# Kernel optimization log

Hardware: AMD Instinct MI355X
Metric: run time of the kernel (lower is better)

The kernel has to match this reference:

```python
import jax, jax.numpy as jnp
import numpy as np

N_NODES = 50000
N_EDGES = 800000
D = 128


def _degrees(idx, n):
    # in/out degree via segment_sum of ones, clamped to >=1 (DGL clamp)
    ones = jnp.ones(idx.shape[0], dtype=jnp.float32)
    return jnp.clip(jax.ops.segment_sum(ones, idx, num_segments=n), 1.0)


def graph_conv(x, src, dst, W, b):
    # DGL GraphConv, norm='both', aggregate-then-matmul (in_feats == out_feats)
    n = x.shape[0]
    deg_out = _degrees(src, n)  # [N]
    deg_in = _degrees(dst, n)   # [N]
    xs = x * jax.lax.rsqrt(deg_out)[:, None]          # [N, D] pre-normalize
    msg = jax.ops.segment_sum(xs[src], dst, num_segments=n)  # gather+scatter [N, D]
    h = msg * jax.lax.rsqrt(deg_in)[:, None]
    return h @ W + b


def setup_inputs() -> dict:
    key = jax.random.key(0)
    k1, k2, k3, k4, k5 = jax.random.split(key, 5)
    x = jax.random.normal(k1, (N_NODES, D), dtype=jnp.float32)
    src = jax.random.randint(k2, (N_EDGES,), 0, N_NODES, dtype=jnp.int64)
    dst = jax.random.randint(k3, (N_EDGES,), 0, N_NODES, dtype=jnp.int64)
    scale = 1.0 / np.sqrt(D)
    W1 = jax.random.normal(k4, (D, D), dtype=jnp.float32) * scale
    W2 = jax.random.normal(k5, (D, D), dtype=jnp.float32) * scale
    b1 = jnp.zeros((D,), dtype=jnp.float32)
    b2 = jnp.zeros((D,), dtype=jnp.float32)
    return {"x": x, "src": src, "dst": dst, "W1": W1, "b1": b1, "W2": W2, "b2": b2}


def reference(x, src, dst, W1, b1, W2, b2):
    h = graph_conv(x, src, dst, W1, b1)
    h = jax.nn.relu(h)
    return graph_conv(h, src, dst, W2, b2)
```

## Files before the change

### kernel.cpp

```cpp
#include <hip/hip_runtime.h>

#define N_NODES 50000
#define N_EDGES 800000
#define D 128
#define CAP 48
#define OVF_CAP 4096

#define BINS 40
#define PNODES 1250
#define B1 64
#define CH1 ((N_EDGES + B1 - 1) / B1)
#define NW (N_NODES / 4)

typedef unsigned short bf16_t;
typedef __attribute__((ext_vector_type(8))) short short8v;
typedef __attribute__((ext_vector_type(4))) float f32x4;

__device__ inline float bf2f(bf16_t u) {
    union { unsigned int i; float f; } v;
    v.i = ((unsigned int)u) << 16;
    return v.f;
}
__device__ inline bf16_t f2bf(float f) {
    union { float f; unsigned int i; } v;
    v.f = f;
    unsigned int u = v.i;
    unsigned int r = (u + 0x7FFFu + ((u >> 16) & 1u)) >> 16;
    return (bf16_t)r;
}
__device__ inline float u2f_lo(unsigned int u) {
    union { unsigned int i; float f; } x; x.i = u << 16; return x.f;
}
__device__ inline float u2f_hi(unsigned int u) {
    union { unsigned int i; float f; } x; x.i = u & 0xFFFF0000u; return x.f;
}


__global__ __launch_bounds__(1024) void hist40_kernel(const int* __restrict__ src,
                                                      const int* __restrict__ dst,
                                                      unsigned int* __restrict__ H40,
                                                      unsigned int* __restrict__ SH, int nE) {
    __shared__ unsigned int hb[BINS];
    __shared__ unsigned int hs[NW];
    for (int i = threadIdx.x; i < NW; i += 1024) hs[i] = 0u;
    if (threadIdx.x < BINS) hb[threadIdx.x] = 0u;
    __syncthreads();
    int e0 = blockIdx.x * CH1;
    int e1 = min(e0 + CH1, nE);
    for (int e = e0 + (int)threadIdx.x; e < e1; e += 1024) {
        int s = src[e];
        int d = dst[e];
        atomicAdd(&hs[s >> 2], 1u << (8 * (s & 3)));
        atomicAdd(&hb[d / PNODES], 1u);
    }
    __syncthreads();
    if (threadIdx.x < BINS) H40[blockIdx.x * BINS + threadIdx.x] = hb[threadIdx.x];
    unsigned int* SHb = SH + (size_t)blockIdx.x * NW;
    for (int i = threadIdx.x; i < NW; i += 1024) SHb[i] = hs[i];
}

__global__ void scan40_kernel(const unsigned int* __restrict__ H40,
                              unsigned int* __restrict__ OFF40,
                              unsigned int* __restrict__ binBase,
                              unsigned int* __restrict__ binTot) {
    __shared__ unsigned int part[B1 * BINS];
    __shared__ unsigned int tot[BINS], base[BINS];
    int j = (int)threadIdx.x;
    if (j < BINS) {
        unsigned int run = 0;
        for (int b = 0; b < B1; b++) {
            part[b * BINS + j] = run;
            run += H40[b * BINS + j];
        }
        tot[j] = run;
    }
    __syncthreads();
    if (j == 0) {
        unsigned int run = 0;
        for (int q = 0; q < BINS; q++) { base[q] = run; run += tot[q]; }
    }
    __syncthreads();
    if (j < BINS) {
        binBase[j] = base[j];
        binTot[j] = tot[j];
        for (int b = 0; b < B1; b++) OFF40[b * BINS + j] = part[b * BINS + j] + base[j];
    }
}

__global__ __launch_bounds__(1024) void place40_kernel(const int* __restrict__ src,
                                                       const int* __restrict__ dst,
                                                       const unsigned int* __restrict__ OFF40,
                                                       unsigned int* __restrict__ binned, int nE) {
    __shared__ unsigned int cur[BINS];
    if (threadIdx.x < BINS) cur[threadIdx.x] = OFF40[blockIdx.x * BINS + threadIdx.x];
    __syncthreads();
    int e0 = blockIdx.x * CH1;
    int e1 = min(e0 + CH1, nE);
    for (int e = e0 + (int)threadIdx.x; e < e1; e += 1024) {
        int s = src[e];
        int d = dst[e];
        int bin = d / PNODES;
        unsigned int pos = atomicAdd(&cur[bin], 1u);
        binned[pos] = (unsigned int)(d - bin * PNODES) | ((unsigned int)s << 16);
    }
}

__global__ void sreduce_kernel(const unsigned int* __restrict__ SH, int* __restrict__ cnt_s) {
    int w = blockIdx.x * 256 + (int)threadIdx.x;
    if (w >= NW) return;
    unsigned int run = 0;
#pragma unroll 8
    for (int b = 0; b < B1; b++) run += SH[(size_t)b * NW + w];
    int4 c;
    c.x = (int)(run & 0xFFu); c.y = (int)((run >> 8) & 0xFFu);
    c.z = (int)((run >> 16) & 0xFFu); c.w = (int)(run >> 24);
    ((int4*)cnt_s)[w] = c;
}

__global__ __launch_bounds__(1024) void scatter2_kernel(
    const unsigned int* __restrict__ binned, const unsigned int* __restrict__ binBase,
    const unsigned int* __restrict__ binTot, unsigned short* __restrict__ bucket,
    int* __restrict__ cnt_d, int* __restrict__ ovf_cnt, int2* __restrict__ ovf) {
    __shared__ unsigned short bk[PNODES * CAP];
    __shared__ unsigned int cur[PNODES];
    const int j = blockIdx.x;
    const int nbeg = j * PNODES;
    for (int i = threadIdx.x; i < PNODES; i += 1024) cur[i] = 0u;
    __syncthreads();
    unsigned int b0 = binBase[j];
    unsigned int n = binTot[j];
    for (unsigned int i = threadIdx.x; i < n; i += 1024) {
        unsigned int v = binned[b0 + i];
        unsigned int dl = v & 0xFFFFu;
        unsigned int s = v >> 16;
        unsigned int q = atomicAdd(&cur[dl], 1u);
        if (q < CAP) {
            bk[dl * CAP + q] = (unsigned short)s;
        } else {
            int o = atomicAdd(ovf_cnt, 1);
            if (o < OVF_CAP) ovf[o] = make_int2(nbeg + (int)dl, (int)s);
        }
    }
    __syncthreads();
    uint4* gb = (uint4*)(bucket + (size_t)nbeg * CAP);
    const uint4* lb = (const uint4*)bk;
    const int n16 = PNODES * CAP * 2 / 16;
    for (int i = threadIdx.x; i < n16; i += 1024) gb[i] = lb[i];
    for (int i = threadIdx.x; i < PNODES; i += 1024) cnt_d[nbeg + i] = (int)cur[i];
}

__global__ void prescale_kernel(const float4* __restrict__ x, const int* __restrict__ cnt_s,
                                const int* __restrict__ cnt_d,
                                float* __restrict__ rs_out, float* __restrict__ rs_in,
                                ushort4* __restrict__ xs4, int nN) {
    int node = blockIdx.x * 8 + (threadIdx.x >> 5);
    int c = threadIdx.x & 31;
    if (node >= nN) return;
    float rs_o = 0.0f;
    if (c == 0) {
        rs_o = rsqrtf(fmaxf((float)cnt_s[node], 1.0f));
        rs_out[node] = rs_o;
        rs_in[node] = rsqrtf(fmaxf((float)cnt_d[node], 1.0f));
    }
    rs_o = __shfl(rs_o, threadIdx.x & 32);
    float4 v = x[(size_t)node * 32 + c];
    ushort4 o;
    o.x = f2bf(v.x * rs_o);
    o.y = f2bf(v.y * rs_o);
    o.z = f2bf(v.z * rs_o);
    o.w = f2bf(v.w * rs_o);
    xs4[(size_t)node * 32 + c] = o;
}

__global__ void gather_kernel(const uint4* __restrict__ xs,
                              const int* __restrict__ cnt_d,
                              const unsigned short* __restrict__ bucket,
                              float4* __restrict__ msg4, int nN) {
    int node = blockIdx.x * 16 + ((int)threadIdx.x >> 4);
    int lane = threadIdx.x & 15;
    if (node >= nN) return;
    const unsigned short* bk = bucket + (size_t)node * CAP;
    int cnt = min(cnt_d[node], CAP);
    float a[8];
#pragma unroll
    for (int k = 0; k < 8; k++) a[k] = 0.f;
#define ACC8(v)                                              \
    a[0] += u2f_lo(v.x); a[1] += u2f_hi(v.x);                \
    a[2] += u2f_lo(v.y); a[3] += u2f_hi(v.y);                \
    a[4] += u2f_lo(v.z); a[5] += u2f_hi(v.z);                \
    a[6] += u2f_lo(v.w); a[7] += u2f_hi(v.w);
    int e = 0;
    for (; e + 3 < cnt; e += 4) {
        int s0 = bk[e], s1 = bk[e + 1], s2 = bk[e + 2], s3 = bk[e + 3];
        uint4 v0 = xs[(size_t)s0 * 16 + lane];
        uint4 v1 = xs[(size_t)s1 * 16 + lane];
        uint4 v2 = xs[(size_t)s2 * 16 + lane];
        uint4 v3 = xs[(size_t)s3 * 16 + lane];
        ACC8(v0) ACC8(v1) ACC8(v2) ACC8(v3)
    }
    for (; e < cnt; e++) {
        int s0 = bk[e];
        uint4 v0 = xs[(size_t)s0 * 16 + lane];
        ACC8(v0)
    }
#undef ACC8
    size_t o = (size_t)node * 32 + lane * 2;
    msg4[o]     = make_float4(a[0], a[1], a[2], a[3]);
    msg4[o + 1] = make_float4(a[4], a[5], a[6], a[7]);
}

__global__ void ovf_kernel(const int2* __restrict__ ovf, const int* __restrict__ ovf_cnt,
                           const ushort4* __restrict__ xs4, float* __restrict__ msg) {
    int n = min(*ovf_cnt, OVF_CAP);
    int lane = threadIdx.x & 31;
    for (int i = (int)(threadIdx.x >> 5); i < n; i += 8) {
        int2 ds = ovf[i];
        ushort4 v = xs4[(size_t)ds.y * 32 + lane];
        float* m = msg + (size_t)ds.x * D + lane * 4;
        atomicAdd(m + 0, bf2f(v.x));
        atomicAdd(m + 1, bf2f(v.y));
        atomicAdd(m + 2, bf2f(v.z));
        atomicAdd(m + 3, bf2f(v.w));
    }
}

__global__ void wsplit_kernel(const float* __restrict__ W1, bf16_t* __restrict__ Wf1,
                              const float* __restrict__ W2, bf16_t* __restrict__ Wf2) {
    const float* W = blockIdx.y ? W2 : W1;
    bf16_t* Wf = blockIdx.y ? Wf2 : Wf1;
    int flat = blockIdx.x * 256 + (int)threadIdx.x;
    int lane = flat & 63;
    int c = (flat >> 6) & 7;
    int ks = flat >> 9;
    int n = c * 16 + (lane & 15);
    int kb = ks * 32 + (lane >> 4) * 8;
#pragma unroll
    for (int j = 0; j < 8; j++) {
        float w = W[(size_t)(kb + j) * D + n];
        bf16_t hi = f2bf(w);
        bf16_t lo = f2bf(w - bf2f(hi));
        Wf[(size_t)flat * 8 + j] = hi;
        Wf[(size_t)(2048 + flat) * 8 + j] = lo;
    }
}

template <bool RELU_OUTSCALE, bool OUT_BF16>
__global__ __launch_bounds__(256) void gemm_mfma_kernel(
    const float* __restrict__ msg, const float* __restrict__ rs_in,
    const float* __restrict__ rs_out, const bf16_t* __restrict__ Wf,
    const float* __restrict__ bias, void* __restrict__ outp, int nN) {
    int lane = (int)threadIdx.x & 63;
    int wave = (int)threadIdx.x >> 6;
    int n0 = blockIdx.x * 64 + wave * 16;
    int ar = lane & 15;
    int kg = lane >> 4;

    short8v ahi[4], alo[4];
    {
        const float* ap = msg + (size_t)(n0 + ar) * D + kg * 8;
        bool valid = (n0 + ar) < nN;
#pragma unroll
        for (int ks = 0; ks < 4; ks++) {
            float av[8];
            if (valid) {
                float4 p0 = *(const float4*)(ap + ks * 32);
                float4 p1 = *(const float4*)(ap + ks * 32 + 4);
                av[0] = p0.x; av[1] = p0.y; av[2] = p0.z; av[3] = p0.w;
                av[4] = p1.x; av[5] = p1.y; av[6] = p1.z; av[7] = p1.w;
            } else {
#pragma unroll
                for (int j = 0; j < 8; j++) av[j] = 0.f;
            }
#pragma unroll
            for (int j = 0; j < 8; j++) {
                bf16_t h = f2bf(av[j]);
                bf16_t l = f2bf(av[j] - bf2f(h));
                ahi[ks][j] = (short)h;
                alo[ks][j] = (short)l;
            }
        }
    }

    f32x4 acc[8];
#pragma unroll
    for (int c = 0; c < 8; c++) acc[c] = (f32x4){0.f, 0.f, 0.f, 0.f};

    const short8v* Bh = (const short8v*)Wf;
    const short8v* Bl = Bh + 2048;
#pragma unroll
    for (int ks = 0; ks < 4; ks++) {
#pragma unroll
        for (int c = 0; c < 8; c++) {
            int off = (ks * 8 + c) * 64 + lane;
            short8v wh = Bh[off];
            short8v wl = Bl[off];
            acc[c] = __builtin_amdgcn_mfma_f32_16x16x32_bf16(ahi[ks], wh, acc[c], 0, 0, 0);
            acc[c] = __builtin_amdgcn_mfma_f32_16x16x32_bf16(alo[ks], wh, acc[c], 0, 0, 0);
            acc[c] = __builtin_amdgcn_mfma_f32_16x16x32_bf16(ahi[ks], wl, acc[c], 0, 0, 0);
        }
    }

    int ocol = lane & 15;
#pragma unroll
    for (int r = 0; r < 4; r++) {
        int node = n0 + kg * 4 + r;
        if (node >= nN) continue;
        float ri = rs_in[node];
        float ro = RELU_OUTSCALE ? rs_out[node] : 1.0f;
#pragma unroll
        for (int c = 0; c < 8; c++) {
            float v = acc[c][r] * ri + bias[c * 16 + ocol];
            if (RELU_OUTSCALE) v = fmaxf(v, 0.0f) * ro;
            if (OUT_BF16) {
                ((bf16_t*)outp)[(size_t)node * D + c * 16 + ocol] = f2bf(v);
            } else {
                ((float*)outp)[(size_t)node * D + c * 16 + ocol] = v;
            }
        }
    }
}

static inline size_t align16(size_t x) { return (x + 15) & ~(size_t)15; }

extern "C" void kernel_launch(void* const* d_in, const int* in_sizes, int n_in,
                              void* d_out, int out_size, void* d_ws, size_t ws_size,
                              hipStream_t stream) {
    const float* x   = (const float*)d_in[0];
    const int*   src = (const int*)d_in[1];
    const int*   dst = (const int*)d_in[2];
    const float* W1  = (const float*)d_in[3];
    const float* b1  = (const float*)d_in[4];
    const float* W2  = (const float*)d_in[5];
    const float* b2  = (const float*)d_in[6];
    float* out = (float*)d_out;

    char* p = (char*)d_ws;
    float*          msg     = (float*)p;          p += align16((size_t)N_NODES * D * sizeof(float));
    int*            cnt_s   = (int*)p;            p += align16(N_NODES * sizeof(int));
    int*            cnt_d   = (int*)p;            p += align16(N_NODES * sizeof(int));
    int*            ovf_cnt = (int*)p;            p += align16(16 * sizeof(int));
    int2*           ovf     = (int2*)p;           p += align16((size_t)OVF_CAP * sizeof(int2));
    unsigned short* bucket  = (unsigned short*)p; p += align16((size_t)N_NODES * CAP * sizeof(unsigned short));
    float*          rs_out  = (float*)p;          p += align16(N_NODES * sizeof(float));
    float*          rs_in   = (float*)p;          p += align16(N_NODES * sizeof(float));
    bf16_t*         Wf1     = (bf16_t*)p;         p += align16((size_t)2 * 2048 * 8 * sizeof(bf16_t));
    bf16_t*         Wf2     = (bf16_t*)p;         p += align16((size_t)2 * 2048 * 8 * sizeof(bf16_t));
    unsigned int*   H40     = (unsigned int*)p;   p += align16((size_t)B1 * BINS * sizeof(unsigned int));
    unsigned int*   OFF40   = (unsigned int*)p;   p += align16((size_t)B1 * BINS * sizeof(unsigned int));
    unsigned int*   binBase = (unsigned int*)p;   p += align16(BINS * sizeof(unsigned int));
    unsigned int*   binTot  = (unsigned int*)p;   p += align16(BINS * sizeof(unsigned int));
    bf16_t*         xs      = (bf16_t*)p;
    bf16_t*         hs      = xs;

    unsigned int* binned = (unsigned int*)msg;
    unsigned int* SH     = binned + N_EDGES;

    hipMemsetAsync(ovf_cnt, 0, 16 * sizeof(int), stream);

    wsplit_kernel<<<dim3(8, 2), 256, 0, stream>>>(W1, Wf1, W2, Wf2);

    hist40_kernel<<<B1, 1024, 0, stream>>>(src, dst, H40, SH, N_EDGES);
    scan40_kernel<<<1, 64, 0, stream>>>(H40, OFF40, binBase, binTot);
    place40_kernel<<<B1, 1024, 0, stream>>>(src, dst, OFF40, binned, N_EDGES);
    sreduce_kernel<<<(NW + 255) / 256, 256, 0, stream>>>(SH, cnt_s);
    scatter2_kernel<<<BINS, 1024, 0, stream>>>(binned, binBase, binTot, bucket,
                                               cnt_d, ovf_cnt, ovf);

    prescale_kernel<<<(N_NODES + 7) / 8, 256, 0, stream>>>((const float4*)x, cnt_s, cnt_d,
                                                           rs_out, rs_in, (ushort4*)xs, N_NODES);

    int ggrid = (N_NODES + 15) / 16;
    int mgrid = (N_NODES + 63) / 64;

    gather_kernel<<<ggrid, 256, 0, stream>>>((const uint4*)xs, cnt_d, bucket,
                                             (float4*)msg, N_NODES);
    ovf_kernel<<<1, 256, 0, stream>>>(ovf, ovf_cnt, (const ushort4*)xs, msg);

    gemm_mfma_kernel<true, true><<<mgrid, 256, 0, stream>>>(
        msg, rs_in, rs_out, Wf1, b1, hs, N_NODES);

    gather_kernel<<<ggrid, 256, 0, stream>>>((const uint4*)hs, cnt_d, bucket,
                                             (float4*)msg, N_NODES);
    ovf_kernel<<<1, 256, 0, stream>>>(ovf, ovf_cnt, (const ushort4*)hs, msg);

    gemm_mfma_kernel<false, false><<<mgrid, 256, 0, stream>>>(
        msg, rs_in, nullptr, Wf2, b2, out, N_NODES);
}
```

Before: 225.4 us.

## Fuse gather, overflow and MFMA GEMM into one kernel per layer

Each layer now gathers neighbor features for a 64-node tile straight into shared memory, applies overflow edges with LDS atomics, and runs the split-bf16 MFMA GEMM from shared memory. This drops the fp32 msg round trip through global memory and the separate gather, ovf and gemm launches. Because of that, xs and hs get separate buffers and binned/SH get their own workspace instead of aliasing msg. The cost is that every block scans the whole overflow list, and the 33KB of LDS per block may lower occupancy during the latency-bound gather.

```diff
diff --git a/kernel.cpp b/kernel.cpp
--- a/kernel.cpp
+++ b/kernel.cpp
@@ -34,7 +34,6 @@
 __device__ inline float u2f_hi(unsigned int u) {
     union { unsigned int i; float f; } x; x.i = u & 0xFFFF0000u; return x.f;
 }
-
 
 __global__ __launch_bounds__(1024) void hist40_kernel(const int* __restrict__ src,
                                                       const int* __restrict__ dst,
@@ -172,58 +171,6 @@
     xs4[(size_t)node * 32 + c] = o;
 }
 
-__global__ void gather_kernel(const uint4* __restrict__ xs,
-                              const int* __restrict__ cnt_d,
-                              const unsigned short* __restrict__ bucket,
-                              float4* __restrict__ msg4, int nN) {
-    int node = blockIdx.x * 16 + ((int)threadIdx.x >> 4);
-    int lane = threadIdx.x & 15;
-    if (node >= nN) return;
-    const unsigned short* bk = bucket + (size_t)node * CAP;
-    int cnt = min(cnt_d[node], CAP);
-    float a[8];
-#pragma unroll
-    for (int k = 0; k < 8; k++) a[k] = 0.f;
-#define ACC8(v)                                              \
-    a[0] += u2f_lo(v.x); a[1] += u2f_hi(v.x);                \
-    a[2] += u2f_lo(v.y); a[3] += u2f_hi(v.y);                \
-    a[4] += u2f_lo(v.z); a[5] += u2f_hi(v.z);                \
-    a[6] += u2f_lo(v.w); a[7] += u2f_hi(v.w);
-    int e = 0;
-    for (; e + 3 < cnt; e += 4) {
-        int s0 = bk[e], s1 = bk[e + 1], s2 = bk[e + 2], s3 = bk[e + 3];
-        uint4 v0 = xs[(size_t)s0 * 16 + lane];
-        uint4 v1 = xs[(size_t)s1 * 16 + lane];
-        uint4 v2 = xs[(size_t)s2 * 16 + lane];
-        uint4 v3 = xs[(size_t)s3 * 16 + lane];
-        ACC8(v0) ACC8(v1) ACC8(v2) ACC8(v3)
-    }
-    for (; e < cnt; e++) {
-        int s0 = bk[e];
-        uint4 v0 = xs[(size_t)s0 * 16 + lane];
-        ACC8(v0)
-    }
-#undef ACC8
-    size_t o = (size_t)node * 32 + lane * 2;
-    msg4[o]     = make_float4(a[0], a[1], a[2], a[3]);
-    msg4[o + 1] = make_float4(a[4], a[5], a[6], a[7]);
-}
-
-__global__ void ovf_kernel(const int2* __restrict__ ovf, const int* __restrict__ ovf_cnt,
-                           const ushort4* __restrict__ xs4, float* __restrict__ msg) {
-    int n = min(*ovf_cnt, OVF_CAP);
-    int lane = threadIdx.x & 31;
-    for (int i = (int)(threadIdx.x >> 5); i < n; i += 8) {
-        int2 ds = ovf[i];
-        ushort4 v = xs4[(size_t)ds.y * 32 + lane];
-        float* m = msg + (size_t)ds.x * D + lane * 4;
-        atomicAdd(m + 0, bf2f(v.x));
-        atomicAdd(m + 1, bf2f(v.y));
-        atomicAdd(m + 2, bf2f(v.z));
-        atomicAdd(m + 3, bf2f(v.w));
-    }
-}
-
 __global__ void wsplit_kernel(const float* __restrict__ W1, bf16_t* __restrict__ Wf1,
                               const float* __restrict__ W2, bf16_t* __restrict__ Wf2) {
     const float* W = blockIdx.y ? W2 : W1;
@@ -244,40 +191,93 @@
     }
 }
 
+#define LDW 132
 template <bool RELU_OUTSCALE, bool OUT_BF16>
-__global__ __launch_bounds__(256) void gemm_mfma_kernel(
-    const float* __restrict__ msg, const float* __restrict__ rs_in,
-    const float* __restrict__ rs_out, const bf16_t* __restrict__ Wf,
-    const float* __restrict__ bias, void* __restrict__ outp, int nN) {
-    int lane = (int)threadIdx.x & 63;
-    int wave = (int)threadIdx.x >> 6;
-    int n0 = blockIdx.x * 64 + wave * 16;
+__global__ __launch_bounds__(256) void fused_layer_kernel(
+    const uint4* __restrict__ xsrc,
+    const int* __restrict__ cnt_d,
+    const unsigned short* __restrict__ bucket,
+    const int* __restrict__ ovf_cnt, const int2* __restrict__ ovf,
+    const float* __restrict__ rs_in, const float* __restrict__ rs_out,
+    const bf16_t* __restrict__ Wf, const float* __restrict__ bias,
+    void* __restrict__ outp, int nN) {
+    __shared__ float sA[64 * LDW];
+    int tid = (int)threadIdx.x;
+    int n0 = blockIdx.x * 64;
+    int lane16 = tid & 15;
+    int grp = tid >> 4;
+
+#define ACC8(v)                                              \
+    a[0] += u2f_lo(v.x); a[1] += u2f_hi(v.x);                \
+    a[2] += u2f_lo(v.y); a[3] += u2f_hi(v.y);                \
+    a[4] += u2f_lo(v.z); a[5] += u2f_hi(v.z);                \
+    a[6] += u2f_lo(v.w); a[7] += u2f_hi(v.w);
+#pragma unroll
+    for (int r = 0; r < 4; r++) {
+        int ln = r * 16 + grp;
+        int node = n0 + ln;
+        float a[8];
+#pragma unroll
+        for (int k = 0; k < 8; k++) a[k] = 0.f;
+        if (node < nN) {
+            const unsigned short* bk = bucket + (size_t)node * CAP;
+            int cnt = min(cnt_d[node], CAP);
+            int e = 0;
+            for (; e + 3 < cnt; e += 4) {
+                int s0 = bk[e], s1 = bk[e + 1], s2 = bk[e + 2], s3 = bk[e + 3];
+                uint4 v0 = xsrc[(size_t)s0 * 16 + lane16];
+                uint4 v1 = xsrc[(size_t)s1 * 16 + lane16];
+                uint4 v2 = xsrc[(size_t)s2 * 16 + lane16];
+                uint4 v3 = xsrc[(size_t)s3 * 16 + lane16];
+                ACC8(v0) ACC8(v1) ACC8(v2) ACC8(v3)
+            }
+            for (; e < cnt; e++) {
+                int s0 = bk[e];
+                uint4 v0 = xsrc[(size_t)s0 * 16 + lane16];
+                ACC8(v0)
+            }
+        }
+        float* row = sA + ln * LDW + lane16 * 8;
+#pragma unroll
+        for (int k = 0; k < 8; k++) row[k] = a[k];
+    }
+#undef ACC8
+
+    int novf = min(*ovf_cnt, OVF_CAP);
+    if (novf > 0) {
+        __syncthreads();
+        for (int i = tid; i < novf; i += 256) {
+            int2 ds = ovf[i];
+            int ln = ds.x - n0;
+            if ((unsigned)ln < 64u) {
+                const uint4* xr = xsrc + (size_t)ds.y * 16;
+                for (int c = 0; c < 16; c++) {
+                    uint4 v = xr[c];
+                    float* q = sA + ln * LDW + c * 8;
+                    atomicAdd(q + 0, u2f_lo(v.x)); atomicAdd(q + 1, u2f_hi(v.x));
+                    atomicAdd(q + 2, u2f_lo(v.y)); atomicAdd(q + 3, u2f_hi(v.y));
+                    atomicAdd(q + 4, u2f_lo(v.z)); atomicAdd(q + 5, u2f_hi(v.z));
+                    atomicAdd(q + 6, u2f_lo(v.w)); atomicAdd(q + 7, u2f_hi(v.w));
+                }
+            }
+        }
+    }
+    __syncthreads();
+
+    int lane = tid & 63;
+    int wave = tid >> 6;
     int ar = lane & 15;
     int kg = lane >> 4;
-
+    const float* ap = sA + (wave * 16 + ar) * LDW + kg * 8;
     short8v ahi[4], alo[4];
-    {
-        const float* ap = msg + (size_t)(n0 + ar) * D + kg * 8;
-        bool valid = (n0 + ar) < nN;
-#pragma unroll
-        for (int ks = 0; ks < 4; ks++) {
-            float av[8];
-            if (valid) {
-                float4 p0 = *(const float4*)(ap + ks * 32);
-                float4 p1 = *(const float4*)(ap + ks * 32 + 4);
-                av[0] = p0.x; av[1] = p0.y; av[2] = p0.z; av[3] = p0.w;
-                av[4] = p1.x; av[5] = p1.y; av[6] = p1.z; av[7] = p1.w;
-            } else {
-#pragma unroll
-                for (int j = 0; j < 8; j++) av[j] = 0.f;
-            }
-#pragma unroll
-            for (int j = 0; j < 8; j++) {
-                bf16_t h = f2bf(av[j]);
-                bf16_t l = f2bf(av[j] - bf2f(h));
-                ahi[ks][j] = (short)h;
-                alo[ks][j] = (short)l;
-            }
+#pragma unroll
+    for (int ks = 0; ks < 4; ks++) {
+#pragma unroll
+        for (int j = 0; j < 8; j++) {
+            float av = ap[ks * 32 + j];
+            bf16_t h = f2bf(av);
+            ahi[ks][j] = (short)h;
+            alo[ks][j] = (short)f2bf(av - bf2f(h));
         }
     }
 
@@ -303,7 +303,7 @@
     int ocol = lane & 15;
 #pragma unroll
     for (int r = 0; r < 4; r++) {
-        int node = n0 + kg * 4 + r;
+        int node = n0 + wave * 16 + kg * 4 + r;
         if (node >= nN) continue;
         float ri = rs_in[node];
         float ro = RELU_OUTSCALE ? rs_out[node] : 1.0f;
@@ -319,6 +319,7 @@
         }
     }
 }
+#undef LDW
 
 static inline size_t align16(size_t x) { return (x + 15) & ~(size_t)15; }
 
@@ -335,7 +336,6 @@
     float* out = (float*)d_out;
 
     char* p = (char*)d_ws;
-    float*          msg     = (float*)p;          p += align16((size_t)N_NODES * D * sizeof(float));
     int*            cnt_s   = (int*)p;            p += align16(N_NODES * sizeof(int));
     int*            cnt_d   = (int*)p;            p += align16(N_NODES * sizeof(int));
     int*            ovf_cnt = (int*)p;            p += align16(16 * sizeof(int));
@@ -349,11 +349,10 @@
     unsigned int*   OFF40   = (unsigned int*)p;   p += align16((size_t)B1 * BINS * sizeof(unsigned int));
     unsigned int*   binBase = (unsigned int*)p;   p += align16(BINS * sizeof(unsigned int));
     unsigned int*   binTot  = (unsigned int*)p;   p += align16(BINS * sizeof(unsigned int));
-    bf16_t*         xs      = (bf16_t*)p;
-    bf16_t*         hs      = xs;
-
-    unsigned int* binned = (unsigned int*)msg;
-    unsigned int* SH     = binned + N_EDGES;
+    unsigned int*   binned  = (unsigned int*)p;   p += align16((size_t)N_EDGES * sizeof(unsigned int));
+    unsigned int*   SH      = (unsigned int*)p;   p += align16((size_t)B1 * NW * sizeof(unsigned int));
+    bf16_t*         xs      = (bf16_t*)p;         p += align16((size_t)N_NODES * D * sizeof(bf16_t));
+    bf16_t*         hs      = (bf16_t*)p;
 
     hipMemsetAsync(ovf_cnt, 0, 16 * sizeof(int), stream);
 
@@ -369,20 +368,11 @@
     prescale_kernel<<<(N_NODES + 7) / 8, 256, 0, stream>>>((const float4*)x, cnt_s, cnt_d,
                                                            rs_out, rs_in, (ushort4*)xs, N_NODES);
 
-    int ggrid = (N_NODES + 15) / 16;
-    int mgrid = (N_NODES + 63) / 64;
-
-    gather_kernel<<<ggrid, 256, 0, stream>>>((const uint4*)xs, cnt_d, bucket,
-                                             (float4*)msg, N_NODES);
-    ovf_kernel<<<1, 256, 0, stream>>>(ovf, ovf_cnt, (const ushort4*)xs, msg);
-
-    gemm_mfma_kernel<true, true><<<mgrid, 256, 0, stream>>>(
-        msg, rs_in, rs_out, Wf1, b1, hs, N_NODES);
-
-    gather_kernel<<<ggrid, 256, 0, stream>>>((const uint4*)hs, cnt_d, bucket,
-                                             (float4*)msg, N_NODES);
-    ovf_kernel<<<1, 256, 0, stream>>>(ovf, ovf_cnt, (const ushort4*)hs, msg);
-
-    gemm_mfma_kernel<false, false><<<mgrid, 256, 0, stream>>>(
-        msg, rs_in, nullptr, Wf2, b2, out, N_NODES);
-}
+    int fgrid = (N_NODES + 63) / 64;
+
+    fused_layer_kernel<true, true><<<fgrid, 256, 0, stream>>>(
+        (const uint4*)xs, cnt_d, bucket, ovf_cnt, ovf, rs_in, rs_out, Wf1, b1, hs, N_NODES);
+
+    fused_layer_kernel<false, false><<<fgrid, 256, 0, stream>>>(
+        (const uint4*)hs, cnt_d, bucket, ovf_cnt, ovf, rs_in, rs_out, Wf2, b2, out, N_NODES);
+}
```

Result: faster. 207.3 us (-8.0%).
